# Performance work log

Measured on AMD Instinct MI355X. Metric: run time of the kernel, lower is better.

## Reference

```python
import jax, jax.numpy as jnp
import numpy as np

EPS = 0.1        # entropic regularization (init eps)
MAX_ITER = 100   # init max_iter
THRESH = 0.1     # early-stop threshold from original code
NORM_EPS = 1e-8


def setup_inputs() -> dict:
    key = jax.random.key(0)
    kx, ky = jax.random.split(key)
    x = jax.random.normal(kx, (16, 1024, 256), dtype=jnp.float32)
    y = jax.random.normal(ky, (16, 1024, 256), dtype=jnp.float32)
    return {"x": x, "y": y}


def _mfa_cost(x, y):
    # Cosine cost: E = 1 - cos(x_i, y_j), computed via normalized matmul
    # (norms clamped at 1e-8 as in torch CosineSimilarity).
    xn = x / jnp.maximum(jnp.linalg.norm(x, axis=-1, keepdims=True), NORM_EPS)
    yn = y / jnp.maximum(jnp.linalg.norm(y, axis=-1, keepdims=True), NORM_EPS)
    E = 1.0 - jnp.einsum('bnd,bmd->bnm', xn, yn)  # [B, N, M]

    B, N, M = E.shape
    log_mu = jnp.full((B, N), jnp.log(1.0 / N + 1e-8), dtype=E.dtype)
    log_nu = jnp.full((B, M), jnp.log(1.0 / M + 1e-8), dtype=E.dtype)

    def Mmat(u, v):
        # (-E + u_i + v_j) / eps, broadcast over [B, N, M]
        return (-E + u[..., :, None] + v[..., None, :]) / EPS

    @jax.checkpoint
    def body(carry, _):
        u, v, done = carry
        u_new = EPS * (log_mu - jax.nn.logsumexp(Mmat(u, v), axis=-1)) + u
        # original transposes then logsumexp over -1 == logsumexp over -2
        v_new = EPS * (log_nu - jax.nn.logsumexp(Mmat(u_new, v), axis=-2)) + v
        err = jnp.abs(u_new - u).sum(-1).mean()
        # emulate data-dependent break: freeze u, v once converged
        u_out = jnp.where(done, u, u_new)
        v_out = jnp.where(done, v, v_new)
        return (u_out, v_out, done | (err < THRESH)), None

    u0 = jnp.zeros((B, N), dtype=E.dtype)
    v0 = jnp.zeros((B, M), dtype=E.dtype)
    (u, v, _), _ = jax.lax.scan(body, (u0, v0, jnp.array(False)), None, length=MAX_ITER)

    pi = jnp.exp(Mmat(u, v))                 # transport plan [B, N, M]
    cost = jnp.sum(pi * E, axis=(-2, -1))    # [B]  (reduction='none')
    return cost


def reference(x, y):
    return _mfa_cost(x, y)
```

## Files before the change

### kernel.cpp

```cpp
#include <hip/hip_runtime.h>

typedef _Float16 half_t;
typedef __attribute__((ext_vector_type(8))) _Float16 half8;
typedef __attribute__((ext_vector_type(4))) float f32x4;
typedef __attribute__((ext_vector_type(8))) short short8v;
typedef unsigned short u16;
typedef unsigned int u32;

#define SCALE_F     14.4269504f
#define INV_SCALE_F 0.0693147181f
#define C_MU       -9.99998523f
#define C_NU       -9.99998523f
#define MU_F        0.000976572498f
#define ERR_STOP_B  1.44269504f
#define MAX_ITER    100
#define SPIN_LIMIT  50000000LL
#define PV0         3.0517578125e-05f

#define SMEM_E   131072
#define SMEM_CP  16384
#define SMEM_PV  4096
#define SMEM_RED 256
#define SMEM_TOTAL (SMEM_E + SMEM_CP + SMEM_PV + SMEM_RED)

#define PSTRIDE  1040
#define PWORDS   (2*16*16*PSTRIDE)

__device__ __forceinline__ float fexp2(float x) { return __builtin_amdgcn_exp2f(x); }
__device__ __forceinline__ float flog2(float x) { return __builtin_amdgcn_logf(x); }
__device__ __forceinline__ float frcp(float x)  { return __builtin_amdgcn_rcpf(x); }

__device__ __forceinline__ u16 f2bf(float f) {
  unsigned u = __float_as_uint(f);
  return (u16)((u + 0x7fffu + ((u >> 16) & 1u)) >> 16);
}
__device__ __forceinline__ u32 agload(const u32* p) {
  return __hip_atomic_load(p, __ATOMIC_RELAXED, __HIP_MEMORY_SCOPE_AGENT);
}
__device__ __forceinline__ void agstore(u32* p, u32 v) {
  __hip_atomic_store(p, v, __ATOMIC_RELAXED, __HIP_MEMORY_SCOPE_AGENT);
}

__global__ __launch_bounds__(256) void mfa_prep(const float* __restrict__ x,
                                                const float* __restrict__ y,
                                                u16* __restrict__ Xn,
                                                u16* __restrict__ Yn,
                                                u32* __restrict__ partials,
                                                float* __restrict__ cost) {
  int g = blockIdx.x * 256 + threadIdx.x;
  if (g < 16) cost[g] = 0.0f;
  #pragma unroll
  for (int j = 0; j < 9; ++j) {
    int idx = (j << 16) + g;
    if (idx < PWORDS) partials[idx] = 0u;
  }

  int wid = g >> 6;
  int lane = threadIdx.x & 63;
  for (int rr = 0; rr < 32; ++rr) {
    int row = wid + (rr << 10);
    const float* src = (row < 16384) ? x + (size_t)row * 256
                                     : y + (size_t)(row - 16384) * 256;
    float4 xa = ((const float4*)src)[lane];
    float ss = xa.x*xa.x + xa.y*xa.y + xa.z*xa.z + xa.w*xa.w;
    #pragma unroll
    for (int off = 32; off; off >>= 1) ss += __shfl_xor(ss, off);
    float inv = 1.0f / fmaxf(sqrtf(ss), 1e-8f);
    ushort4 o;
    o.x = f2bf(xa.x * inv); o.y = f2bf(xa.y * inv);
    o.z = f2bf(xa.z * inv); o.w = f2bf(xa.w * inv);
    u16* dst = ((row < 16384) ? Xn + ((size_t)row << 8)
                              : Yn + ((size_t)(row - 16384) << 8)) + lane * 4;
    *(ushort4*)dst = o;
  }
}

__global__ __launch_bounds__(512, 1) void mfa_sink_fused(
    const u16* __restrict__ Xn, const u16* __restrict__ Yn,
    u32* __restrict__ partials, float* __restrict__ cost) {
  extern __shared__ char smem[];
  half_t* pEls = (half_t*)smem;
  float*  cpb  = (float*)(smem + SMEM_E);
  float*  pvsh = (float*)(smem + SMEM_E + SMEM_CP);
  float*  sred = (float*)(smem + SMEM_E + SMEM_CP + SMEM_PV);

  const int t = threadIdx.x, w = t >> 6, lane = t & 63;
  const int lane15 = lane & 15, lgrp = lane >> 4;
  const int blk = blockIdx.x;
  const int b = ((blk & 7) << 1) | ((blk >> 7) & 1);
  const int k = (blk >> 3) & 15;

  {
    const u16* Xb = Xn + ((size_t)((b << 10) + (k << 6)) << 8);
    const u16* Yb = Yn + ((size_t)(b << 10) << 8);
    const int wcol = w << 7;
    #pragma unroll
    for (int pass = 0; pass < 2; ++pass) {
      const int c0 = wcol + (pass << 6);
      f32x4 acc[4][4];
      #pragma unroll
      for (int i = 0; i < 4; ++i)
        #pragma unroll
        for (int j = 0; j < 4; ++j) acc[i][j] = (f32x4){0.f, 0.f, 0.f, 0.f};
      for (int ks = 0; ks < 8; ++ks) {
        const int koff = (ks << 5) + (lgrp << 3);
        short8v a[4], bb[4];
        #pragma unroll
        for (int i = 0; i < 4; ++i)
          a[i] = *(const short8v*)(Xb + (((i << 4) + lane15) << 8) + koff);
        #pragma unroll
        for (int j = 0; j < 4; ++j)
          bb[j] = *(const short8v*)(Yb + ((size_t)(c0 + (j << 4) + lane15) << 8) + koff);
        #pragma unroll
        for (int i = 0; i < 4; ++i)
          #pragma unroll
          for (int j = 0; j < 4; ++j)
            acc[i][j] = __builtin_amdgcn_mfma_f32_16x16x32_bf16(a[i], bb[j], acc[i][j], 0, 0, 0);
      }
      #pragma unroll
      for (int i = 0; i < 4; ++i)
        #pragma unroll
        for (int j = 0; j < 4; ++j) {
          const int col = c0 + (j << 4) + lane15;
          #pragma unroll
          for (int q = 0; q < 4; ++q) {
            const int row = (i << 4) + (lgrp << 2) + q;
            pEls[(row << 10) + col] =
                (half_t)fexp2(15.0f - (1.0f - acc[i][j][q]) * SCALE_F);
          }
        }
    }
  }
  pvsh[t] = PV0; pvsh[t + 512] = PV0;
  __syncthreads();

  float ureg[8];
  #pragma unroll
  for (int r = 0; r < 8; ++r) ureg[r] = 0.0f;
  float vr0 = 0.0f, vr1 = 0.0f;

  const int mlo = lane << 3;
  int it = 0;
  for (; it < MAX_ITER; ++it) {
    const f32x4* p4 = (const f32x4*)pvsh;
    f32x4 a4 = p4[lane*2], b4 = p4[lane*2 + 1];
    f32x4 c4 = p4[128 + lane*2], d4 = p4[128 + lane*2 + 1];
    float pv[16];
    pv[0]=a4.x; pv[1]=a4.y; pv[2]=a4.z; pv[3]=a4.w;
    pv[4]=b4.x; pv[5]=b4.y; pv[6]=b4.z; pv[7]=b4.w;
    pv[8]=c4.x; pv[9]=c4.y; pv[10]=c4.z; pv[11]=c4.w;
    pv[12]=d4.x; pv[13]=d4.y; pv[14]=d4.z; pv[15]=d4.w;

    float s[8];
    #pragma unroll
    for (int r = 0; r < 8; ++r) {
      const half8* E8 = (const half8*)(pEls + (((w << 3) + r) << 10));
      half8 ea = E8[lane], eb = E8[lane + 64];
      float acc = 0.0f;
      #pragma unroll
      for (int j = 0; j < 8; ++j) acc = __builtin_fmaf(pv[j], (float)ea[j], acc);
      #pragma unroll
      for (int j = 0; j < 8; ++j) acc = __builtin_fmaf(pv[8+j], (float)eb[j], acc);
      s[r] = acc;
    }
    #pragma unroll
    for (int off = 32; off; off >>= 1) {
      #pragma unroll
      for (int r = 0; r < 8; ++r) s[r] += __shfl_xor(s[r], off);
    }
    float eu[8], werr = 0.0f;
    #pragma unroll
    for (int r = 0; r < 8; ++r) {
      float unew = C_MU - flog2(s[r]);
      eu[r] = MU_F * frcp(s[r]);
      werr += fabsf(unew - ureg[r]);
      ureg[r] = unew;
    }
    if (lane == 0) sred[w] = werr;
    float inner[16];
    #pragma unroll
    for (int j = 0; j < 16; ++j) inner[j] = 0.0f;
    #pragma unroll
    for (int r = 0; r < 8; ++r) {
      const half8* E8 = (const half8*)(pEls + (((w << 3) + r) << 10));
      half8 ea = E8[lane], eb = E8[lane + 64];
      #pragma unroll
      for (int j = 0; j < 8; ++j) inner[j] = __builtin_fmaf((float)ea[j], eu[r], inner[j]);
      #pragma unroll
      for (int j = 0; j < 8; ++j) inner[8+j] = __builtin_fmaf((float)eb[j], eu[r], inner[8+j]);
    }
    float colacc[16];
    #pragma unroll
    for (int j = 0; j < 16; ++j) colacc[j] = inner[j] * pv[j];

    if (w < 4) {
      #pragma unroll
      for (int j = 0; j < 4; ++j) {
        *(f32x4*)&cpb[w*1024 + mlo + 4*j - ((j>=2)?8:0) + ((j>=2)?512:0)] =
            (f32x4){colacc[4*j], colacc[4*j+1], colacc[4*j+2], colacc[4*j+3]};
      }
    }
    __syncthreads();
    if (w >= 4) {
      const int wb = (w - 4) * 1024;
      #pragma unroll
      for (int j = 0; j < 8; ++j) cpb[wb + mlo + j] += colacc[j];
      #pragma unroll
      for (int j = 0; j < 8; ++j) cpb[wb + 512 + mlo + j] += colacc[8 + j];
    }
    __syncthreads();

    const int p = it & 1;
    const u32 tag = (u32)((it + 1) & 3);
    {
      u32* ps = partials + (size_t)((((p << 4) | b) << 4) | k) * PSTRIDE;
      float fa = cpb[t] + cpb[1024 + t] + cpb[2048 + t] + cpb[3072 + t];
      float fb = cpb[512 + t] + cpb[1536 + t] + cpb[2560 + t] + cpb[3584 + t];
      agstore(&ps[t],       (__float_as_uint(fa) & ~3u) | tag);
      agstore(&ps[512 + t], (__float_as_uint(fb) & ~3u) | tag);
      if (t == 0) {
        float be = sred[0]+sred[1]+sred[2]+sred[3]+sred[4]+sred[5]+sred[6]+sred[7];
        agstore(&ps[1024], (__float_as_uint(be) & ~3u) | tag);
      }
    }

    {
      const u32* pr = partials + (size_t)(((p << 4) | b) << 4) * PSTRIDE;
      u32 wa[16], wb[16], wwe = tag;
      long long tws = clock64();
      for (;;) {
        #pragma unroll
        for (int j = 0; j < 16; ++j) {
          wa[j] = agload(&pr[j * PSTRIDE + t]);
          wb[j] = agload(&pr[j * PSTRIDE + 512 + t]);
        }
        u32 diff = 0;
        #pragma unroll
        for (int j = 0; j < 16; ++j)
          diff |= ((wa[j] ^ tag) | (wb[j] ^ tag)) & 3u;
        if (w == 0 && lane < 16) {
          wwe = agload(&pr[lane * PSTRIDE + 1024]);
          diff |= (wwe ^ tag) & 3u;
        }
        if (__all(diff == 0)) break;
        if (clock64() - tws > SPIN_LIMIT) break;
      }
      float t0s = 0.0f, t1s = 0.0f;
      #pragma unroll
      for (int j = 0; j < 16; ++j) {
        t0s += __uint_as_float(wa[j] & ~3u);
        t1s += __uint_as_float(wb[j] & ~3u);
      }
      if (w == 0) {
        float we = __uint_as_float(wwe & ~3u);
        #pragma unroll
        for (int off = 8; off; off >>= 1) we += __shfl_xor(we, off);
        if (lane == 0) sred[8] = we;
      }
      vr0 += C_NU - flog2(t0s);
      vr1 += C_NU - flog2(t1s);
      pvsh[t]       = fexp2(vr0 - 15.0f);
      pvsh[t + 512] = fexp2(vr1 - 15.0f);
    }
    __syncthreads();

    if (sred[8] < ERR_STOP_B) break;
  }

  {
    const f32x4* p4 = (const f32x4*)pvsh;
    f32x4 a4 = p4[lane*2], b4 = p4[lane*2 + 1];
    f32x4 c4 = p4[128 + lane*2], d4 = p4[128 + lane*2 + 1];
    float pv[16];
    pv[0]=a4.x; pv[1]=a4.y; pv[2]=a4.z; pv[3]=a4.w;
    pv[4]=b4.x; pv[5]=b4.y; pv[6]=b4.z; pv[7]=b4.w;
    pv[8]=c4.x; pv[9]=c4.y; pv[10]=c4.z; pv[11]=c4.w;
    pv[12]=d4.x; pv[13]=d4.y; pv[14]=d4.z; pv[15]=d4.w;
    float cacc = 0.0f;
    #pragma unroll
    for (int r = 0; r < 8; ++r) {
      const half8* E8 = (const half8*)(pEls + (((w << 3) + r) << 10));
      half8 ea = E8[lane], eb = E8[lane + 64];
      float su = fexp2(ureg[r]);
      #pragma unroll
      for (int j = 0; j < 8; ++j) {
        float pe = (float)ea[j];
        float e = 15.0f - flog2(pe);
        cacc += su * pv[j] * pe * e;
      }
      #pragma unroll
      for (int j = 0; j < 8; ++j) {
        float pe = (float)eb[j];
        float e = 15.0f - flog2(pe);
        cacc += su * pv[8 + j] * pe * e;
      }
    }
    #pragma unroll
    for (int off = 32; off; off >>= 1) cacc += __shfl_xor(cacc, off);
    if (lane == 0) sred[w] = cacc;
    __syncthreads();
    if (t == 0)
      atomicAdd(&cost[b], (sred[0]+sred[1]+sred[2]+sred[3]+sred[4]+sred[5]+
                           sred[6]+sred[7]) * INV_SCALE_F);
  }
}

extern "C" void kernel_launch(void* const* d_in, const int* in_sizes, int n_in,
                              void* d_out, int out_size, void* d_ws, size_t ws_size,
                              hipStream_t stream) {
  const float* x = (const float*)d_in[0];
  const float* y = (const float*)d_in[1];
  float* cost = (float*)d_out;

  char* base = (char*)d_ws;
  u16* Xn       = (u16*)base;
  u16* Yn       = (u16*)(base + 8388608);
  u32* partials = (u32*)(base + 16777216);
  size_t needed = 16777216 + (size_t)PWORDS * 4;
  if (ws_size < needed) return;

  mfa_prep<<<256, 256, 0, stream>>>(x, y, Xn, Yn, partials, cost);

  (void)hipFuncSetAttribute((const void*)mfa_sink_fused,
                            hipFuncAttributeMaxDynamicSharedMemorySize, SMEM_TOTAL);
  mfa_sink_fused<<<dim3(256), dim3(512), SMEM_TOTAL, stream>>>(
      Xn, Yn, partials, cost);
}
```

Before: 74.71 us.

## Double block to 1024 threads and reduce column sums via LDS atomics

Doubles the threads per block from 512 to 1024, so each wave owns 4 rows instead of 8 and each thread handles a single column in the cross-block exchange. The column-partial reduction now uses swizzled shared-memory float atomics into a single 1024-entry buffer instead of a two-phase store/add across four buffers, which shrinks LDS usage. The E rows are held in registers between the row-sum and column-sum passes to avoid re-reading LDS. The intent is more latency hiding and shorter per-thread serial chains, at the risk of LDS atomic contention, higher register pressure under the 1024-thread launch bound, and a non-deterministic summation order.

```diff
diff --git a/kernel.cpp b/kernel.cpp
--- a/kernel.cpp
+++ b/kernel.cpp
@@ -18,13 +18,15 @@
 #define PV0         3.0517578125e-05f
 
 #define SMEM_E   131072
-#define SMEM_CP  16384
+#define SMEM_CP  4096
 #define SMEM_PV  4096
 #define SMEM_RED 256
 #define SMEM_TOTAL (SMEM_E + SMEM_CP + SMEM_PV + SMEM_RED)
 
 #define PSTRIDE  1040
 #define PWORDS   (2*16*16*PSTRIDE)
+
+#define SWZ(c) ((c) ^ (((c) >> 5) & 7))
 
 __device__ __forceinline__ float fexp2(float x) { return __builtin_amdgcn_exp2f(x); }
 __device__ __forceinline__ float flog2(float x) { return __builtin_amdgcn_logf(x); }
@@ -75,7 +77,7 @@
   }
 }
 
-__global__ __launch_bounds__(512, 1) void mfa_sink_fused(
+__global__ __launch_bounds__(1024, 1) void mfa_sink_fused(
     const u16* __restrict__ Xn, const u16* __restrict__ Yn,
     u32* __restrict__ partials, float* __restrict__ cost) {
   extern __shared__ char smem[];
@@ -93,34 +95,33 @@
   {
     const u16* Xb = Xn + ((size_t)((b << 10) + (k << 6)) << 8);
     const u16* Yb = Yn + ((size_t)(b << 10) << 8);
-    const int wcol = w << 7;
     #pragma unroll
     for (int pass = 0; pass < 2; ++pass) {
-      const int c0 = wcol + (pass << 6);
-      f32x4 acc[4][4];
+      const int c0 = (w << 6) + (pass << 5);
+      f32x4 acc[4][2];
       #pragma unroll
       for (int i = 0; i < 4; ++i)
         #pragma unroll
-        for (int j = 0; j < 4; ++j) acc[i][j] = (f32x4){0.f, 0.f, 0.f, 0.f};
+        for (int j = 0; j < 2; ++j) acc[i][j] = (f32x4){0.f, 0.f, 0.f, 0.f};
       for (int ks = 0; ks < 8; ++ks) {
         const int koff = (ks << 5) + (lgrp << 3);
-        short8v a[4], bb[4];
+        short8v a[4], bb[2];
         #pragma unroll
         for (int i = 0; i < 4; ++i)
           a[i] = *(const short8v*)(Xb + (((i << 4) + lane15) << 8) + koff);
         #pragma unroll
-        for (int j = 0; j < 4; ++j)
+        for (int j = 0; j < 2; ++j)
           bb[j] = *(const short8v*)(Yb + ((size_t)(c0 + (j << 4) + lane15) << 8) + koff);
         #pragma unroll
         for (int i = 0; i < 4; ++i)
           #pragma unroll
-          for (int j = 0; j < 4; ++j)
+          for (int j = 0; j < 2; ++j)
             acc[i][j] = __builtin_amdgcn_mfma_f32_16x16x32_bf16(a[i], bb[j], acc[i][j], 0, 0, 0);
       }
       #pragma unroll
       for (int i = 0; i < 4; ++i)
         #pragma unroll
-        for (int j = 0; j < 4; ++j) {
+        for (int j = 0; j < 2; ++j) {
           const int col = c0 + (j << 4) + lane15;
           #pragma unroll
           for (int q = 0; q < 4; ++q) {
@@ -131,15 +132,15 @@
         }
     }
   }
-  pvsh[t] = PV0; pvsh[t + 512] = PV0;
+  pvsh[t] = PV0;
+  cpb[t]  = 0.0f;
   __syncthreads();
 
-  float ureg[8];
+  float ureg[4];
   #pragma unroll
-  for (int r = 0; r < 8; ++r) ureg[r] = 0.0f;
-  float vr0 = 0.0f, vr1 = 0.0f;
-
-  const int mlo = lane << 3;
+  for (int r = 0; r < 4; ++r) ureg[r] = 0.0f;
+  float vr = 0.0f;
+
   int it = 0;
   for (; it < MAX_ITER; ++it) {
     const f32x4* p4 = (const f32x4*)pvsh;
@@ -151,62 +152,53 @@
     pv[8]=c4.x; pv[9]=c4.y; pv[10]=c4.z; pv[11]=c4.w;
     pv[12]=d4.x; pv[13]=d4.y; pv[14]=d4.z; pv[15]=d4.w;
 
-    float s[8];
-    #pragma unroll
-    for (int r = 0; r < 8; ++r) {
-      const half8* E8 = (const half8*)(pEls + (((w << 3) + r) << 10));
-      half8 ea = E8[lane], eb = E8[lane + 64];
+    half8 ea[4], eb[4];
+    float s[4];
+    #pragma unroll
+    for (int r = 0; r < 4; ++r) {
+      const half8* E8 = (const half8*)(pEls + (((w << 2) + r) << 10));
+      ea[r] = E8[lane]; eb[r] = E8[lane + 64];
       float acc = 0.0f;
       #pragma unroll
-      for (int j = 0; j < 8; ++j) acc = __builtin_fmaf(pv[j], (float)ea[j], acc);
-      #pragma unroll
-      for (int j = 0; j < 8; ++j) acc = __builtin_fmaf(pv[8+j], (float)eb[j], acc);
+      for (int j = 0; j < 8; ++j) acc = __builtin_fmaf(pv[j], (float)ea[r][j], acc);
+      #pragma unroll
+      for (int j = 0; j < 8; ++j) acc = __builtin_fmaf(pv[8+j], (float)eb[r][j], acc);
       s[r] = acc;
     }
     #pragma unroll
     for (int off = 32; off; off >>= 1) {
       #pragma unroll
-      for (int r = 0; r < 8; ++r) s[r] += __shfl_xor(s[r], off);
-    }
-    float eu[8], werr = 0.0f;
-    #pragma unroll
-    for (int r = 0; r < 8; ++r) {
+      for (int r = 0; r < 4; ++r) s[r] += __shfl_xor(s[r], off);
+    }
+    float eu[4], werr = 0.0f;
+    #pragma unroll
+    for (int r = 0; r < 4; ++r) {
       float unew = C_MU - flog2(s[r]);
       eu[r] = MU_F * frcp(s[r]);
       werr += fabsf(unew - ureg[r]);
       ureg[r] = unew;
     }
     if (lane == 0) sred[w] = werr;
-    float inner[16];
-    #pragma unroll
-    for (int j = 0; j < 16; ++j) inner[j] = 0.0f;
-    #pragma unroll
-    for (int r = 0; r < 8; ++r) {
-      const half8* E8 = (const half8*)(pEls + (((w << 3) + r) << 10));
-      half8 ea = E8[lane], eb = E8[lane + 64];
-      #pragma unroll
-      for (int j = 0; j < 8; ++j) inner[j] = __builtin_fmaf((float)ea[j], eu[r], inner[j]);
-      #pragma unroll
-      for (int j = 0; j < 8; ++j) inner[8+j] = __builtin_fmaf((float)eb[j], eu[r], inner[8+j]);
-    }
-    float colacc[16];
-    #pragma unroll
-    for (int j = 0; j < 16; ++j) colacc[j] = inner[j] * pv[j];
-
-    if (w < 4) {
-      #pragma unroll
-      for (int j = 0; j < 4; ++j) {
-        *(f32x4*)&cpb[w*1024 + mlo + 4*j - ((j>=2)?8:0) + ((j>=2)?512:0)] =
-            (f32x4){colacc[4*j], colacc[4*j+1], colacc[4*j+2], colacc[4*j+3]};
-      }
-    }
-    __syncthreads();
-    if (w >= 4) {
-      const int wb = (w - 4) * 1024;
-      #pragma unroll
-      for (int j = 0; j < 8; ++j) cpb[wb + mlo + j] += colacc[j];
-      #pragma unroll
-      for (int j = 0; j < 8; ++j) cpb[wb + 512 + mlo + j] += colacc[8 + j];
+    {
+      float inner[16];
+      #pragma unroll
+      for (int j = 0; j < 16; ++j) inner[j] = 0.0f;
+      #pragma unroll
+      for (int r = 0; r < 4; ++r) {
+        #pragma unroll
+        for (int j = 0; j < 8; ++j)
+          inner[j] = __builtin_fmaf((float)ea[r][j], eu[r], inner[j]);
+        #pragma unroll
+        for (int j = 0; j < 8; ++j)
+          inner[8+j] = __builtin_fmaf((float)eb[r][j], eu[r], inner[8+j]);
+      }
+      const int cb0 = lane << 3;
+      #pragma unroll
+      for (int j = 0; j < 8; ++j)
+        atomicAdd(&cpb[SWZ(cb0 + j)], inner[j] * pv[j]);
+      #pragma unroll
+      for (int j = 0; j < 8; ++j)
+        atomicAdd(&cpb[SWZ(512 + cb0 + j)], inner[8+j] * pv[8+j]);
     }
     __syncthreads();
 
@@ -214,30 +206,27 @@
     const u32 tag = (u32)((it + 1) & 3);
     {
       u32* ps = partials + (size_t)((((p << 4) | b) << 4) | k) * PSTRIDE;
-      float fa = cpb[t] + cpb[1024 + t] + cpb[2048 + t] + cpb[3072 + t];
-      float fb = cpb[512 + t] + cpb[1536 + t] + cpb[2560 + t] + cpb[3584 + t];
-      agstore(&ps[t],       (__float_as_uint(fa) & ~3u) | tag);
-      agstore(&ps[512 + t], (__float_as_uint(fb) & ~3u) | tag);
+      float fa = cpb[SWZ(t)];
+      agstore(&ps[t], (__float_as_uint(fa) & ~3u) | tag);
       if (t == 0) {
-        float be = sred[0]+sred[1]+sred[2]+sred[3]+sred[4]+sred[5]+sred[6]+sred[7];
+        float be = 0.0f;
+        #pragma unroll
+        for (int j = 0; j < 16; ++j) be += sred[j];
         agstore(&ps[1024], (__float_as_uint(be) & ~3u) | tag);
       }
     }
 
     {
       const u32* pr = partials + (size_t)(((p << 4) | b) << 4) * PSTRIDE;
-      u32 wa[16], wb[16], wwe = tag;
+      u32 wv[16], wwe = tag;
       long long tws = clock64();
       for (;;) {
         #pragma unroll
-        for (int j = 0; j < 16; ++j) {
-          wa[j] = agload(&pr[j * PSTRIDE + t]);
-          wb[j] = agload(&pr[j * PSTRIDE + 512 + t]);
-        }
+        for (int j = 0; j < 16; ++j)
+          wv[j] = agload(&pr[j * PSTRIDE + t]);
         u32 diff = 0;
         #pragma unroll
-        for (int j = 0; j < 16; ++j)
-          diff |= ((wa[j] ^ tag) | (wb[j] ^ tag)) & 3u;
+        for (int j = 0; j < 16; ++j) diff |= (wv[j] ^ tag) & 3u;
         if (w == 0 && lane < 16) {
           wwe = agload(&pr[lane * PSTRIDE + 1024]);
           diff |= (wwe ^ tag) & 3u;
@@ -245,26 +234,22 @@
         if (__all(diff == 0)) break;
         if (clock64() - tws > SPIN_LIMIT) break;
       }
-      float t0s = 0.0f, t1s = 0.0f;
-      #pragma unroll
-      for (int j = 0; j < 16; ++j) {
-        t0s += __uint_as_float(wa[j] & ~3u);
-        t1s += __uint_as_float(wb[j] & ~3u);
-      }
+      float ts = 0.0f;
+      #pragma unroll
+      for (int j = 0; j < 16; ++j) ts += __uint_as_float(wv[j] & ~3u);
       if (w == 0) {
-        float we = __uint_as_float(wwe & ~3u);
+        float we = (lane < 16) ? __uint_as_float(wwe & ~3u) : 0.0f;
         #pragma unroll
         for (int off = 8; off; off >>= 1) we += __shfl_xor(we, off);
-        if (lane == 0) sred[8] = we;
-      }
-      vr0 += C_NU - flog2(t0s);
-      vr1 += C_NU - flog2(t1s);
-      pvsh[t]       = fexp2(vr0 - 15.0f);
-      pvsh[t + 512] = fexp2(vr1 - 15.0f);
+        if (lane == 0) sred[16] = we;
+      }
+      vr += C_NU - flog2(ts);
+      pvsh[t] = fexp2(vr - 15.0f);
+      cpb[SWZ(t)] = 0.0f;
     }
     __syncthreads();
 
-    if (sred[8] < ERR_STOP_B) break;
+    if (sred[16] < ERR_STOP_B) break;
   }
 
   {
@@ -278,8 +263,8 @@
     pv[12]=d4.x; pv[13]=d4.y; pv[14]=d4.z; pv[15]=d4.w;
     float cacc = 0.0f;
     #pragma unroll
-    for (int r = 0; r < 8; ++r) {
-      const half8* E8 = (const half8*)(pEls + (((w << 3) + r) << 10));
+    for (int r = 0; r < 4; ++r) {
+      const half8* E8 = (const half8*)(pEls + (((w << 2) + r) << 10));
       half8 ea = E8[lane], eb = E8[lane + 64];
       float su = fexp2(ureg[r]);
       #pragma unroll
@@ -299,9 +284,12 @@
     for (int off = 32; off; off >>= 1) cacc += __shfl_xor(cacc, off);
     if (lane == 0) sred[w] = cacc;
     __syncthreads();
-    if (t == 0)
-      atomicAdd(&cost[b], (sred[0]+sred[1]+sred[2]+sred[3]+sred[4]+sred[5]+
-                           sred[6]+sred[7]) * INV_SCALE_F);
+    if (t == 0) {
+      float csum = 0.0f;
+      #pragma unroll
+      for (int j = 0; j < 16; ++j) csum += sred[j];
+      atomicAdd(&cost[b], csum * INV_SCALE_F);
+    }
   }
 }
 
@@ -323,6 +311,6 @@
 
   (void)hipFuncSetAttribute((const void*)mfa_sink_fused,
                             hipFuncAttributeMaxDynamicSharedMemorySize, SMEM_TOTAL);
-  mfa_sink_fused<<<dim3(256), dim3(512), SMEM_TOTAL, stream>>>(
+  mfa_sink_fused<<<dim3(256), dim3(1024), SMEM_TOTAL, stream>>>(
       Xn, Yn, partials, cost);
 }
```

Result: slower. 132.4 us (+77.3%).
